# Performance work log

Measured on AMD Instinct MI355X. Metric: run time of the kernel, lower is better.

## Reference

```python
import jax, jax.numpy as jnp
import numpy as np

N = 50000        # nodes
E = 800000       # edges (avg degree 16)
NODE_DIM = 64
HID = 64
OUT = 1
K = 2            # hops per TAGConv
P = 0.5          # dropout rate


def setup_inputs() -> dict:
    key = jax.random.key(0)
    ks = jax.random.split(key, 8)
    x = jax.random.normal(ks[0], (N, NODE_DIM), dtype=jnp.float32)
    edge_index = jax.random.randint(ks[1], (2, E), 0, N, dtype=jnp.int64)
    # positive edge weights (traffic-style), keeps degree normalization well-defined
    edge_attr = jax.random.uniform(ks[2], (E,), dtype=jnp.float32, minval=0.1, maxval=1.0)
    s = 0.1
    W0 = (jax.random.normal(ks[3], (K + 1, NODE_DIM, HID), dtype=jnp.float32) * s)
    W1 = (jax.random.normal(ks[4], (K + 1, HID, HID), dtype=jnp.float32) * s)
    W2 = (jax.random.normal(ks[5], (K + 1, HID, OUT), dtype=jnp.float32) * s)
    a0 = jnp.full((1,), 0.25, dtype=jnp.float32)  # PReLU slope (num_parameters=1)
    a1 = jnp.full((1,), 0.25, dtype=jnp.float32)
    return {"x": x, "edge_index": edge_index, "edge_attr": edge_attr,
            "W0": W0, "W1": W1, "W2": W2, "a0": a0, "a1": a1}


def _tagconv(x, row, col, norm, W):
    # out = sum_{k=0..K} (A_norm^k x) @ W[k]
    out = x @ W[0]
    h = x
    for k in range(1, K + 1):
        # gather source features, scale by edge norm, scatter-add to targets
        h = jax.ops.segment_sum(h[row] * norm[:, None], col, num_segments=N)
        out = out + h @ W[k]
    return out


def _dropout(h, key):
    keep = jax.random.bernoulli(key, 1.0 - P, h.shape)
    return jnp.where(keep, h / (1.0 - P), 0.0)


def _prelu(h, a):
    return jnp.where(h >= 0, h, a * h)


def reference(x, edge_index, edge_attr, W0, W1, W2, a0, a1):
    row, col = edge_index[0], edge_index[1]
    # symmetric GCN normalization (PyG TAGConv default, no added self-loops)
    deg = jax.ops.segment_sum(edge_attr, col, num_segments=N)
    dinv = jnp.where(deg > 0, jax.lax.rsqrt(jnp.maximum(deg, 1e-12)), 0.0)
    norm = dinv[row] * edge_attr * dinv[col]

    dk = jax.random.split(jax.random.key(42), 2)
    h = _tagconv(x, row, col, norm, W0)
    h = _prelu(_dropout(h, dk[0]), a0)
    h = _tagconv(h, row, col, norm, W1)
    h = _prelu(_dropout(h, dk[1]), a1)
    return _tagconv(h, row, col, norm, W2)
```

## Files before the change

### kernel.cpp

```cpp
#include <hip/hip_runtime.h>
#include <stdint.h>

#define N_NODES 50000
#define N_EDGES 800000
#define DIM 64
#define FEAT_TOTAL (N_NODES * DIM)
#define ELL_S 48
#define NB 200
#define BROWS 250
#define BCAP 6000
#define ECHUNK (N_EDGES / NB)
#define AST 200

typedef __attribute__((ext_vector_type(8))) short bf16x8;
typedef __attribute__((ext_vector_type(4))) float f32x4;

__device__ inline float bf2f(uint32_t h) { return __uint_as_float(h << 16); }
__device__ inline uint32_t f2bf(float f) {
  uint32_t u = __float_as_uint(f);
  return (u + 0x7fffu + ((u >> 16) & 1u)) >> 16;
}

__host__ __device__ inline void threefry2x32(uint32_t k0, uint32_t k1,
                                             uint32_t x0, uint32_t x1,
                                             uint32_t& o0, uint32_t& o1) {
  uint32_t ks[3] = {k0, k1, k0 ^ k1 ^ 0x1BD11BDAu};
  x0 += ks[0];
  x1 += ks[1];
  const uint32_t R[2][4] = {{13u, 15u, 26u, 6u}, {17u, 29u, 16u, 24u}};
#pragma unroll
  for (int g = 0; g < 5; ++g) {
    const uint32_t* r = R[g & 1];
#pragma unroll
    for (int j = 0; j < 4; ++j) {
      x0 += x1;
      x1 = (x1 << r[j]) | (x1 >> (32u - r[j]));
      x1 ^= x0;
    }
    x0 += ks[(g + 1) % 3];
    x1 += ks[(g + 2) % 3] + (uint32_t)(g + 1);
  }
  o0 = x0;
  o1 = x1;
}

__global__ __launch_bounds__(256) void phaseA(
    const int* __restrict__ row, const int* __restrict__ col,
    const float* __restrict__ w, int* __restrict__ bfill,
    int2* __restrict__ bkt, int E) {
  __shared__ int hist[NB], base[NB], off[NB];
  int t = threadIdx.x;
  int lo = blockIdx.x * ECHUNK;
  int hi = min(lo + ECHUNK, E);
  for (int i = t; i < NB; i += 256) hist[i] = 0;
  __syncthreads();
  for (int e = lo + t; e < hi; e += 256) atomicAdd(&hist[col[e] / BROWS], 1);
  __syncthreads();
  for (int i = t; i < NB; i += 256) {
    base[i] = atomicAdd(&bfill[i], hist[i]);
    off[i] = 0;
  }
  __syncthreads();
  for (int e = lo + t; e < hi; e += 256) {
    int c = col[e];
    int bin = c / BROWS;
    int rank = atomicAdd(&off[bin], 1);
    int dest = base[bin] + rank;
    if (dest < BCAP) {
      int2 ent;
      ent.x = row[e] | ((c - bin * BROWS) << 17);
      ent.y = __float_as_int(w[e]);
      bkt[(size_t)bin * BCAP + dest] = ent;
    }
  }
}

__global__ __launch_bounds__(256) void phaseC(
    const int* __restrict__ bfill, const int2* __restrict__ bkt,
    int2* __restrict__ ell, int* __restrict__ cnt, float* __restrict__ deg) {
  __shared__ int lcnt[BROWS];
  __shared__ float ldeg[BROWS];
  int t = threadIdx.x;
  int b = blockIdx.x;
  for (int i = t; i < BROWS; i += 256) {
    lcnt[i] = 0;
    ldeg[i] = 0.0f;
  }
  __syncthreads();
  int sz = min(bfill[b], BCAP);
  const int2* src = bkt + (size_t)b * BCAP;
  for (int i = t; i < sz; i += 256) {
    int2 ent = src[i];
    int cl = (ent.x >> 17) & 0xff;
    int r = ent.x & 0x1ffff;
    float wv = __int_as_float(ent.y);
    int slot = atomicAdd(&lcnt[cl], 1);
    if (slot < ELL_S) {
      int2 o;
      o.x = r;
      o.y = ent.y;
      ell[(size_t)(b * BROWS + cl) * ELL_S + slot] = o;
    }
    atomicAdd(&ldeg[cl], wv);
  }
  __syncthreads();
  for (int i = t; i < BROWS; i += 256) {
    cnt[b * BROWS + i] = lcnt[i];
    deg[b * BROWS + i] = ldeg[i];
  }
}

__global__ void dinv_kernel(float* __restrict__ d_io, int n) {
  int i = blockIdx.x * blockDim.x + threadIdx.x;
  if (i >= n) return;
  float d = d_io[i];
  d_io[i] = (d > 0.0f) ? rsqrtf(fmaxf(d, 1e-12f)) : 0.0f;
}

__global__ void normw_ell(int2* __restrict__ ell, const int* __restrict__ cnt,
                          const float* __restrict__ dinv, int n_nodes) {
  int gid = blockIdx.x * blockDim.x + threadIdx.x;
  int n = gid >> 6;
  if (n >= n_nodes) return;
  int lane = threadIdx.x & 63;
  int c = min(cnt[n], ELL_S);
  if (lane >= c) return;
  float dn = dinv[n];
  int2 ent = ell[(size_t)n * ELL_S + lane];
  ent.y = __float_as_int(dinv[ent.x] * __int_as_float(ent.y) * dn);
  ell[(size_t)n * ELL_S + lane] = ent;
}

__global__ void cvt_wt(const float* __restrict__ W0, const float* __restrict__ W1,
                       uint16_t* __restrict__ Wt0, uint16_t* __restrict__ Wt1) {
  int id = blockIdx.x * blockDim.x + threadIdx.x;
  if (id >= 192 * DIM) return;
  int kk = id >> 6;
  int j = id & 63;
  Wt0[j * 192 + kk] = (uint16_t)f2bf(W0[id]);
  Wt1[j * 192 + kk] = (uint16_t)f2bf(W1[id]);
}

__global__ void prop_f32(const float* __restrict__ src,
                         uint16_t* __restrict__ dst,
                         const int2* __restrict__ ell,
                         const int* __restrict__ cnt, int n_nodes) {
  int gid = blockIdx.x * blockDim.x + threadIdx.x;
  int n = gid >> 6;
  if (n >= n_nodes) return;
  int lane = threadIdx.x & 63;
  int eg = lane >> 4;
  int fc = lane & 15;
  int c = min(cnt[n], ELL_S);
  const int2* p = ell + (size_t)n * ELL_S;
  float4 acc = {0.f, 0.f, 0.f, 0.f};
  int k = eg;
  for (; k + 4 < c; k += 8) {
    int2 e0 = p[k];
    int2 e1 = p[k + 4];
    float w0 = __int_as_float(e0.y);
    float w1 = __int_as_float(e1.y);
    float4 v0 = *(const float4*)&src[e0.x * DIM + fc * 4];
    float4 v1 = *(const float4*)&src[e1.x * DIM + fc * 4];
    acc.x += v0.x * w0 + v1.x * w1;
    acc.y += v0.y * w0 + v1.y * w1;
    acc.z += v0.z * w0 + v1.z * w1;
    acc.w += v0.w * w0 + v1.w * w1;
  }
  if (k < c) {
    int2 e0 = p[k];
    float w0 = __int_as_float(e0.y);
    float4 v = *(const float4*)&src[e0.x * DIM + fc * 4];
    acc.x += v.x * w0;
    acc.y += v.y * w0;
    acc.z += v.z * w0;
    acc.w += v.w * w0;
  }
#pragma unroll
  for (int m = 16; m <= 32; m <<= 1) {
    acc.x += __shfl_xor(acc.x, m);
    acc.y += __shfl_xor(acc.y, m);
    acc.z += __shfl_xor(acc.z, m);
    acc.w += __shfl_xor(acc.w, m);
  }
  if (eg == 0) {
    uint2 r;
    r.x = f2bf(acc.x) | (f2bf(acc.y) << 16);
    r.y = f2bf(acc.z) | (f2bf(acc.w) << 16);
    *(uint2*)&dst[(size_t)n * DIM + fc * 4] = r;
  }
}

__global__ void prop_bf16(const uint16_t* __restrict__ src,
                          uint16_t* __restrict__ dst,
                          const int2* __restrict__ ell,
                          const int* __restrict__ cnt, int n_nodes) {
  int gid = blockIdx.x * blockDim.x + threadIdx.x;
  int n = gid >> 5;
  if (n >= n_nodes) return;
  int hl = threadIdx.x & 31;
  int eg = hl >> 3;
  int fc = hl & 7;
  int c = min(cnt[n], ELL_S);
  const int2* p = ell + (size_t)n * ELL_S;
  float acc[8] = {0.f, 0.f, 0.f, 0.f, 0.f, 0.f, 0.f, 0.f};
  int k = eg;
  for (; k + 4 < c; k += 8) {
    int2 e0 = p[k];
    int2 e1 = p[k + 4];
    float w0 = __int_as_float(e0.y);
    float w1 = __int_as_float(e1.y);
    uint4 v0 = *(const uint4*)&src[e0.x * DIM + fc * 8];
    uint4 v1 = *(const uint4*)&src[e1.x * DIM + fc * 8];
    acc[0] += bf2f(v0.x & 0xffffu) * w0 + bf2f(v1.x & 0xffffu) * w1;
    acc[1] += bf2f(v0.x >> 16) * w0 + bf2f(v1.x >> 16) * w1;
    acc[2] += bf2f(v0.y & 0xffffu) * w0 + bf2f(v1.y & 0xffffu) * w1;
    acc[3] += bf2f(v0.y >> 16) * w0 + bf2f(v1.y >> 16) * w1;
    acc[4] += bf2f(v0.z & 0xffffu) * w0 + bf2f(v1.z & 0xffffu) * w1;
    acc[5] += bf2f(v0.z >> 16) * w0 + bf2f(v1.z >> 16) * w1;
    acc[6] += bf2f(v0.w & 0xffffu) * w0 + bf2f(v1.w & 0xffffu) * w1;
    acc[7] += bf2f(v0.w >> 16) * w0 + bf2f(v1.w >> 16) * w1;
  }
  if (k < c) {
    int2 e0 = p[k];
    float w0 = __int_as_float(e0.y);
    uint4 v0 = *(const uint4*)&src[e0.x * DIM + fc * 8];
    acc[0] += bf2f(v0.x & 0xffffu) * w0;
    acc[1] += bf2f(v0.x >> 16) * w0;
    acc[2] += bf2f(v0.y & 0xffffu) * w0;
    acc[3] += bf2f(v0.y >> 16) * w0;
    acc[4] += bf2f(v0.z & 0xffffu) * w0;
    acc[5] += bf2f(v0.z >> 16) * w0;
    acc[6] += bf2f(v0.w & 0xffffu) * w0;
    acc[7] += bf2f(v0.w >> 16) * w0;
  }
#pragma unroll
  for (int m = 8; m <= 16; m <<= 1) {
#pragma unroll
    for (int j = 0; j < 8; ++j) acc[j] += __shfl_xor(acc[j], m);
  }
  if (eg == 0) {
    uint4 r;
    r.x = f2bf(acc[0]) | (f2bf(acc[1]) << 16);
    r.y = f2bf(acc[2]) | (f2bf(acc[3]) << 16);
    r.z = f2bf(acc[4]) | (f2bf(acc[5]) << 16);
    r.w = f2bf(acc[6]) | (f2bf(acc[7]) << 16);
    *(uint4*)&dst[(size_t)n * DIM + fc * 8] = r;
  }
}

__global__ void sprop_add_ell(const float* __restrict__ src,
                              const float* __restrict__ addv,
                              float* __restrict__ dst,
                              const int2* __restrict__ ell,
                              const int* __restrict__ cnt, int n_nodes) {
  int n = blockIdx.x * blockDim.x + threadIdx.x;
  if (n >= n_nodes) return;
  int c = min(cnt[n], ELL_S);
  const int2* p = ell + (size_t)n * ELL_S;
  float acc = addv[n];
  for (int k = 0; k < c; ++k)
    acc += __int_as_float(p[k].y) * src[p[k].x];
  dst[n] = acc;
}

template <bool XF32>
__global__ __launch_bounds__(256) void gemm3_mfma(
    const void* Xv, const uint16_t* __restrict__ P1,
    const uint16_t* __restrict__ P2, const uint16_t* __restrict__ Wt,
    uint16_t* out, int n_nodes, uint32_t k0, uint32_t k1,
    const float* __restrict__ a) {
  __shared__ uint16_t sA[64 * AST];
  __shared__ uint16_t sB[64 * AST];
  int t = threadIdx.x;
  int n0 = blockIdx.x * 64;
  if (XF32) {
    const float* X = (const float*)Xv;
#pragma unroll
    for (int it = 0; it < 2; ++it) {
      int chunk = t + it * 256;
      int rrow = chunk >> 3;
      int cc = chunk & 7;
      int nc = min(n0 + rrow, n_nodes - 1);
      const float* s = &X[(size_t)nc * DIM + cc * 8];
      float4 v0 = *(const float4*)s;
      float4 v1 = *(const float4*)(s + 4);
      uint16_t* d = &sA[rrow * AST + cc * 8];
      d[0] = (uint16_t)f2bf(v0.x);
      d[1] = (uint16_t)f2bf(v0.y);
      d[2] = (uint16_t)f2bf(v0.z);
      d[3] = (uint16_t)f2bf(v0.w);
      d[4] = (uint16_t)f2bf(v1.x);
      d[5] = (uint16_t)f2bf(v1.y);
      d[6] = (uint16_t)f2bf(v1.z);
      d[7] = (uint16_t)f2bf(v1.w);
    }
  } else {
    const uint16_t* X = (const uint16_t*)Xv;
#pragma unroll
    for (int it = 0; it < 2; ++it) {
      int chunk = t + it * 256;
      int rrow = chunk >> 3;
      int cc = chunk & 7;
      int nc = min(n0 + rrow, n_nodes - 1);
      uint4 v = *(const uint4*)&X[(size_t)nc * DIM + cc * 8];
      *(uint4*)&sA[rrow * AST + cc * 8] = v;
    }
  }
#pragma unroll
  for (int m = 1; m < 3; ++m) {
    const uint16_t* S = (m == 1) ? P1 : P2;
#pragma unroll
    for (int it = 0; it < 2; ++it) {
      int chunk = t + it * 256;
      int rrow = chunk >> 3;
      int cc = chunk & 7;
      int nc = min(n0 + rrow, n_nodes - 1);
      uint4 v = *(const uint4*)&S[(size_t)nc * DIM + cc * 8];
      *(uint4*)&sA[rrow * AST + m * DIM + cc * 8] = v;
    }
  }
#pragma unroll
  for (int it = 0; it < 6; ++it) {
    int chunk = t + it * 256;
    int rrow = chunk / 24;
    int cc = chunk % 24;
    uint4 v = *(const uint4*)&Wt[rrow * 192 + cc * 8];
    *(uint4*)&sB[rrow * AST + cc * 8] = v;
  }
  __syncthreads();
  int wv = t >> 6;
  int lane = t & 63;
  int lm = lane & 15;
  int quad = lane >> 4;
  f32x4 acc[4] = {};
  const uint16_t* pB = &sB[(wv * 16 + lm) * AST + quad * 8];
  const uint16_t* pA = &sA[lm * AST + quad * 8];
#pragma unroll
  for (int ks = 0; ks < 6; ++ks) {
    bf16x8 bf = *(const bf16x8*)(pB + ks * 32);
#pragma unroll
    for (int rt = 0; rt < 4; ++rt) {
      bf16x8 af = *(const bf16x8*)(pA + rt * 16 * AST + ks * 32);
      acc[rt] = __builtin_amdgcn_mfma_f32_16x16x32_bf16(af, bf, acc[rt], 0, 0, 0);
    }
  }
  float al = a[0];
  int col = wv * 16 + lm;
#pragma unroll
  for (int rt = 0; rt < 4; ++rt) {
#pragma unroll
    for (int r = 0; r < 4; ++r) {
      int n = n0 + rt * 16 + quad * 4 + r;
      if (n < n_nodes) {
        float v = acc[rt][r];
        uint32_t idx = (uint32_t)(n * DIM + col);
        uint32_t o0, o1;
        threefry2x32(k0, k1, 0u, idx, o0, o1);
        v = ((o0 ^ o1) & 0x80000000u) ? 0.0f : (v + v);
        v = (v >= 0.0f) ? v : al * v;
        out[(size_t)n * DIM + col] = (uint16_t)f2bf(v);
      }
    }
  }
}

__global__ void matvec3_bf16(const uint16_t* __restrict__ F,
                             const float* __restrict__ W2,
                             float* __restrict__ y0, float* __restrict__ y1,
                             float* __restrict__ y2, int n_nodes) {
  int gid = blockIdx.x * blockDim.x + threadIdx.x;
  int n = gid >> 6;
  int i = gid & 63;
  if (n >= n_nodes) return;
  float v = bf2f((uint32_t)F[(size_t)n * DIM + i]);
  float s0 = v * W2[i], s1 = v * W2[DIM + i], s2 = v * W2[2 * DIM + i];
#pragma unroll
  for (int off = 32; off > 0; off >>= 1) {
    s0 += __shfl_down(s0, off);
    s1 += __shfl_down(s1, off);
    s2 += __shfl_down(s2, off);
  }
  if (i == 0) {
    y0[n] = s0;
    y1[n] = s1;
    y2[n] = s2;
  }
}

extern "C" void kernel_launch(void* const* d_in, const int* in_sizes, int n_in,
                              void* d_out, int out_size, void* d_ws,
                              size_t ws_size, hipStream_t stream) {
  const float* x = (const float*)d_in[0];
  const int* ei = (const int*)d_in[1];
  const float* ew = (const float*)d_in[2];
  const float* W0 = (const float*)d_in[3];
  const float* W1 = (const float*)d_in[4];
  const float* W2 = (const float*)d_in[5];
  const float* a0 = (const float*)d_in[6];
  const float* a1 = (const float*)d_in[7];
  float* out = (float*)d_out;

  const int* row = ei;
  const int* col = ei + N_EDGES;

  const size_t need = (size_t)(2 * N_NODES + 256) * 4 +
                      (size_t)NB * BCAP * 8 + (size_t)N_NODES * ELL_S * 8 +
                      (size_t)(2 * 192 * DIM) * 2 +
                      (size_t)(3 * FEAT_TOTAL) * 2 + (size_t)(4 * N_NODES) * 4;
  if (ws_size < need) return;
  float* deg = (float*)d_ws;
  int* cnt = (int*)(deg + N_NODES);
  int* bfill = cnt + N_NODES;
  int2* bkt = (int2*)(bfill + 256);
  int2* ell = bkt + (size_t)NB * BCAP;
  uint16_t* Wt0 = (uint16_t*)(ell + (size_t)N_NODES * ELL_S);
  uint16_t* Wt1 = Wt0 + 192 * DIM;
  uint16_t* F0 = Wt1 + 192 * DIM;
  uint16_t* F1 = F0 + FEAT_TOTAL;
  uint16_t* F2 = F1 + FEAT_TOTAL;
  float* y0 = (float*)(F2 + FEAT_TOTAL);
  float* y1 = y0 + N_NODES;
  float* y2 = y1 + N_NODES;
  float* z1 = y2 + N_NODES;

  uint32_t dk0_0, dk0_1, dk1_0, dk1_1;
  threefry2x32(0u, 42u, 0u, 0u, dk0_0, dk0_1);
  threefry2x32(0u, 42u, 0u, 1u, dk1_0, dk1_1);

  const int BLK = 256;
  const int gridN = (N_NODES + BLK - 1) / BLK;
  const int gridNF = (FEAT_TOTAL + BLK - 1) / BLK;
  const int gridNH = (N_NODES * 32 + BLK - 1) / BLK;
  const int gridT = (N_NODES + 63) / 64;

  hipMemsetAsync(bfill, 0, 256 * sizeof(int), stream);
  phaseA<<<NB, BLK, 0, stream>>>(row, col, ew, bfill, bkt, N_EDGES);
  phaseC<<<NB, BLK, 0, stream>>>(bfill, bkt, ell, cnt, deg);
  dinv_kernel<<<gridN, BLK, 0, stream>>>(deg, N_NODES);
  normw_ell<<<gridNF, BLK, 0, stream>>>(ell, cnt, deg, N_NODES);
  cvt_wt<<<48, BLK, 0, stream>>>(W0, W1, Wt0, Wt1);

  prop_f32<<<gridNF, BLK, 0, stream>>>(x, F1, ell, cnt, N_NODES);
  prop_bf16<<<gridNH, BLK, 0, stream>>>(F1, F2, ell, cnt, N_NODES);
  gemm3_mfma<true><<<gridT, BLK, 0, stream>>>(x, F1, F2, Wt0, F0, N_NODES,
                                              dk0_0, dk0_1, a0);
  prop_bf16<<<gridNH, BLK, 0, stream>>>(F0, F1, ell, cnt, N_NODES);
  prop_bf16<<<gridNH, BLK, 0, stream>>>(F1, F2, ell, cnt, N_NODES);
  gemm3_mfma<false><<<gridT, BLK, 0, stream>>>(F0, F1, F2, Wt1, F0, N_NODES,
                                               dk1_0, dk1_1, a1);
  matvec3_bf16<<<gridNF, BLK, 0, stream>>>(F0, W2, y0, y1, y2, N_NODES);
  sprop_add_ell<<<gridN, BLK, 0, stream>>>(y2, y1, z1, ell, cnt, N_NODES);
  sprop_add_ell<<<gridN, BLK, 0, stream>>>(z1, y0, out, ell, cnt, N_NODES);
}
```

Before: 262.7 us.

## Fuse second-hop gather into MFMA GEMM and pre-convert input features to bf16

The second propagation hop of each TAGConv layer now runs inside the GEMM kernel. Each block gathers its 64 nodes' neighbour features straight into shared memory, so the F2 buffer is never written to or read back from global memory and one launch per layer disappears. The input x is converted to bf16 up front so the first hop can reuse the bf16 propagation kernel instead of the fp32 one. The dinv computation is folded into phaseC and the weight conversion is merged with the x conversion. In exchange, the gather inside the GEMM runs with far fewer threads and an LDS-heavy block, so its latency hiding may be weaker than in the standalone propagation kernel.

After: 301.5 us. 1.15x slower.

```diff
diff --git a/kernel.cpp b/kernel.cpp
--- a/kernel.cpp
+++ b/kernel.cpp
@@ -77,7 +77,7 @@
 
 __global__ __launch_bounds__(256) void phaseC(
     const int* __restrict__ bfill, const int2* __restrict__ bkt,
-    int2* __restrict__ ell, int* __restrict__ cnt, float* __restrict__ deg) {
+    int2* __restrict__ ell, int* __restrict__ cnt, float* __restrict__ dinv) {
   __shared__ int lcnt[BROWS];
   __shared__ float ldeg[BROWS];
   int t = threadIdx.x;
@@ -106,15 +106,9 @@
   __syncthreads();
   for (int i = t; i < BROWS; i += 256) {
     cnt[b * BROWS + i] = lcnt[i];
-    deg[b * BROWS + i] = ldeg[i];
-  }
-}
-
-__global__ void dinv_kernel(float* __restrict__ d_io, int n) {
-  int i = blockIdx.x * blockDim.x + threadIdx.x;
-  if (i >= n) return;
-  float d = d_io[i];
-  d_io[i] = (d > 0.0f) ? rsqrtf(fmaxf(d, 1e-12f)) : 0.0f;
+    float d = ldeg[i];
+    dinv[b * BROWS + i] = (d > 0.0f) ? rsqrtf(fmaxf(d, 1e-12f)) : 0.0f;
+  }
 }
 
 __global__ void normw_ell(int2* __restrict__ ell, const int* __restrict__ cnt,
@@ -131,63 +125,18 @@
   ell[(size_t)n * ELL_S + lane] = ent;
 }
 
-__global__ void cvt_wt(const float* __restrict__ W0, const float* __restrict__ W1,
-                       uint16_t* __restrict__ Wt0, uint16_t* __restrict__ Wt1) {
+__global__ void cvt_all(const float* __restrict__ x,
+                        const float* __restrict__ W0,
+                        const float* __restrict__ W1,
+                        uint16_t* __restrict__ xb, uint16_t* __restrict__ Wt0,
+                        uint16_t* __restrict__ Wt1) {
   int id = blockIdx.x * blockDim.x + threadIdx.x;
-  if (id >= 192 * DIM) return;
-  int kk = id >> 6;
-  int j = id & 63;
-  Wt0[j * 192 + kk] = (uint16_t)f2bf(W0[id]);
-  Wt1[j * 192 + kk] = (uint16_t)f2bf(W1[id]);
-}
-
-__global__ void prop_f32(const float* __restrict__ src,
-                         uint16_t* __restrict__ dst,
-                         const int2* __restrict__ ell,
-                         const int* __restrict__ cnt, int n_nodes) {
-  int gid = blockIdx.x * blockDim.x + threadIdx.x;
-  int n = gid >> 6;
-  if (n >= n_nodes) return;
-  int lane = threadIdx.x & 63;
-  int eg = lane >> 4;
-  int fc = lane & 15;
-  int c = min(cnt[n], ELL_S);
-  const int2* p = ell + (size_t)n * ELL_S;
-  float4 acc = {0.f, 0.f, 0.f, 0.f};
-  int k = eg;
-  for (; k + 4 < c; k += 8) {
-    int2 e0 = p[k];
-    int2 e1 = p[k + 4];
-    float w0 = __int_as_float(e0.y);
-    float w1 = __int_as_float(e1.y);
-    float4 v0 = *(const float4*)&src[e0.x * DIM + fc * 4];
-    float4 v1 = *(const float4*)&src[e1.x * DIM + fc * 4];
-    acc.x += v0.x * w0 + v1.x * w1;
-    acc.y += v0.y * w0 + v1.y * w1;
-    acc.z += v0.z * w0 + v1.z * w1;
-    acc.w += v0.w * w0 + v1.w * w1;
-  }
-  if (k < c) {
-    int2 e0 = p[k];
-    float w0 = __int_as_float(e0.y);
-    float4 v = *(const float4*)&src[e0.x * DIM + fc * 4];
-    acc.x += v.x * w0;
-    acc.y += v.y * w0;
-    acc.z += v.z * w0;
-    acc.w += v.w * w0;
-  }
-#pragma unroll
-  for (int m = 16; m <= 32; m <<= 1) {
-    acc.x += __shfl_xor(acc.x, m);
-    acc.y += __shfl_xor(acc.y, m);
-    acc.z += __shfl_xor(acc.z, m);
-    acc.w += __shfl_xor(acc.w, m);
-  }
-  if (eg == 0) {
-    uint2 r;
-    r.x = f2bf(acc.x) | (f2bf(acc.y) << 16);
-    r.y = f2bf(acc.z) | (f2bf(acc.w) << 16);
-    *(uint2*)&dst[(size_t)n * DIM + fc * 4] = r;
+  if (id < FEAT_TOTAL) xb[id] = (uint16_t)f2bf(x[id]);
+  if (id < 192 * DIM) {
+    int kk = id >> 6;
+    int j = id & 63;
+    Wt0[j * 192 + kk] = (uint16_t)f2bf(W0[id]);
+    Wt1[j * 192 + kk] = (uint16_t)f2bf(W1[id]);
   }
 }
 
@@ -264,52 +213,18 @@
   dst[n] = acc;
 }
 
-template <bool XF32>
-__global__ __launch_bounds__(256) void gemm3_mfma(
-    const void* Xv, const uint16_t* __restrict__ P1,
-    const uint16_t* __restrict__ P2, const uint16_t* __restrict__ Wt,
-    uint16_t* out, int n_nodes, uint32_t k0, uint32_t k1,
-    const float* __restrict__ a) {
+__global__ __launch_bounds__(256) void gemm3_mfma_g(
+    const uint16_t* X, const uint16_t* __restrict__ P1,
+    const int2* __restrict__ ell, const int* __restrict__ cnt,
+    const uint16_t* __restrict__ Wt, uint16_t* out, int n_nodes, uint32_t k0,
+    uint32_t k1, const float* __restrict__ a) {
   __shared__ uint16_t sA[64 * AST];
   __shared__ uint16_t sB[64 * AST];
   int t = threadIdx.x;
   int n0 = blockIdx.x * 64;
-  if (XF32) {
-    const float* X = (const float*)Xv;
-#pragma unroll
-    for (int it = 0; it < 2; ++it) {
-      int chunk = t + it * 256;
-      int rrow = chunk >> 3;
-      int cc = chunk & 7;
-      int nc = min(n0 + rrow, n_nodes - 1);
-      const float* s = &X[(size_t)nc * DIM + cc * 8];
-      float4 v0 = *(const float4*)s;
-      float4 v1 = *(const float4*)(s + 4);
-      uint16_t* d = &sA[rrow * AST + cc * 8];
-      d[0] = (uint16_t)f2bf(v0.x);
-      d[1] = (uint16_t)f2bf(v0.y);
-      d[2] = (uint16_t)f2bf(v0.z);
-      d[3] = (uint16_t)f2bf(v0.w);
-      d[4] = (uint16_t)f2bf(v1.x);
-      d[5] = (uint16_t)f2bf(v1.y);
-      d[6] = (uint16_t)f2bf(v1.z);
-      d[7] = (uint16_t)f2bf(v1.w);
-    }
-  } else {
-    const uint16_t* X = (const uint16_t*)Xv;
-#pragma unroll
-    for (int it = 0; it < 2; ++it) {
-      int chunk = t + it * 256;
-      int rrow = chunk >> 3;
-      int cc = chunk & 7;
-      int nc = min(n0 + rrow, n_nodes - 1);
-      uint4 v = *(const uint4*)&X[(size_t)nc * DIM + cc * 8];
-      *(uint4*)&sA[rrow * AST + cc * 8] = v;
-    }
-  }
-#pragma unroll
-  for (int m = 1; m < 3; ++m) {
-    const uint16_t* S = (m == 1) ? P1 : P2;
+#pragma unroll
+  for (int m = 0; m < 2; ++m) {
+    const uint16_t* S = (m == 0) ? X : P1;
 #pragma unroll
     for (int it = 0; it < 2; ++it) {
       int chunk = t + it * 256;
@@ -318,6 +233,65 @@
       int nc = min(n0 + rrow, n_nodes - 1);
       uint4 v = *(const uint4*)&S[(size_t)nc * DIM + cc * 8];
       *(uint4*)&sA[rrow * AST + m * DIM + cc * 8] = v;
+    }
+  }
+  {
+    int wv = t >> 6;
+    int lane = t & 63;
+    int half = lane >> 5;
+    int hl = lane & 31;
+    int eg = hl >> 3;
+    int fc = hl & 7;
+#pragma unroll
+    for (int i = 0; i < 8; ++i) {
+      int ln = wv * 16 + i * 2 + half;
+      int nc = min(n0 + ln, n_nodes - 1);
+      int c = min(cnt[nc], ELL_S);
+      const int2* p = ell + (size_t)nc * ELL_S;
+      float acc[8] = {0.f, 0.f, 0.f, 0.f, 0.f, 0.f, 0.f, 0.f};
+      int k = eg;
+      for (; k + 4 < c; k += 8) {
+        int2 e0 = p[k];
+        int2 e1 = p[k + 4];
+        float w0 = __int_as_float(e0.y);
+        float w1 = __int_as_float(e1.y);
+        uint4 v0 = *(const uint4*)&P1[e0.x * DIM + fc * 8];
+        uint4 v1 = *(const uint4*)&P1[e1.x * DIM + fc * 8];
+        acc[0] += bf2f(v0.x & 0xffffu) * w0 + bf2f(v1.x & 0xffffu) * w1;
+        acc[1] += bf2f(v0.x >> 16) * w0 + bf2f(v1.x >> 16) * w1;
+        acc[2] += bf2f(v0.y & 0xffffu) * w0 + bf2f(v1.y & 0xffffu) * w1;
+        acc[3] += bf2f(v0.y >> 16) * w0 + bf2f(v1.y >> 16) * w1;
+        acc[4] += bf2f(v0.z & 0xffffu) * w0 + bf2f(v1.z & 0xffffu) * w1;
+        acc[5] += bf2f(v0.z >> 16) * w0 + bf2f(v1.z >> 16) * w1;
+        acc[6] += bf2f(v0.w & 0xffffu) * w0 + bf2f(v1.w & 0xffffu) * w1;
+        acc[7] += bf2f(v0.w >> 16) * w0 + bf2f(v1.w >> 16) * w1;
+      }
+      if (k < c) {
+        int2 e0 = p[k];
+        float w0 = __int_as_float(e0.y);
+        uint4 v0 = *(const uint4*)&P1[e0.x * DIM + fc * 8];
+        acc[0] += bf2f(v0.x & 0xffffu) * w0;
+        acc[1] += bf2f(v0.x >> 16) * w0;
+        acc[2] += bf2f(v0.y & 0xffffu) * w0;
+        acc[3] += bf2f(v0.y >> 16) * w0;
+        acc[4] += bf2f(v0.z & 0xffffu) * w0;
+        acc[5] += bf2f(v0.z >> 16) * w0;
+        acc[6] += bf2f(v0.w & 0xffffu) * w0;
+        acc[7] += bf2f(v0.w >> 16) * w0;
+      }
+#pragma unroll
+      for (int m = 8; m <= 16; m <<= 1) {
+#pragma unroll
+        for (int j = 0; j < 8; ++j) acc[j] += __shfl_xor(acc[j], m);
+      }
+      if (eg == 0) {
+        uint4 r;
+        r.x = f2bf(acc[0]) | (f2bf(acc[1]) << 16);
+        r.y = f2bf(acc[2]) | (f2bf(acc[3]) << 16);
+        r.z = f2bf(acc[4]) | (f2bf(acc[5]) << 16);
+        r.w = f2bf(acc[6]) | (f2bf(acc[7]) << 16);
+        *(uint4*)&sA[ln * AST + 2 * DIM + fc * 8] = r;
+      }
     }
   }
 #pragma unroll
@@ -409,17 +383,17 @@
                       (size_t)(2 * 192 * DIM) * 2 +
                       (size_t)(3 * FEAT_TOTAL) * 2 + (size_t)(4 * N_NODES) * 4;
   if (ws_size < need) return;
-  float* deg = (float*)d_ws;
-  int* cnt = (int*)(deg + N_NODES);
+  float* dinv = (float*)d_ws;
+  int* cnt = (int*)(dinv + N_NODES);
   int* bfill = cnt + N_NODES;
   int2* bkt = (int2*)(bfill + 256);
   int2* ell = bkt + (size_t)NB * BCAP;
   uint16_t* Wt0 = (uint16_t*)(ell + (size_t)N_NODES * ELL_S);
   uint16_t* Wt1 = Wt0 + 192 * DIM;
-  uint16_t* F0 = Wt1 + 192 * DIM;
+  uint16_t* xb = Wt1 + 192 * DIM;
+  uint16_t* F0 = xb + FEAT_TOTAL;
   uint16_t* F1 = F0 + FEAT_TOTAL;
-  uint16_t* F2 = F1 + FEAT_TOTAL;
-  float* y0 = (float*)(F2 + FEAT_TOTAL);
+  float* y0 = (float*)(F1 + FEAT_TOTAL);
   float* y1 = y0 + N_NODES;
   float* y2 = y1 + N_NODES;
   float* z1 = y2 + N_NODES;
@@ -436,19 +410,16 @@
 
   hipMemsetAsync(bfill, 0, 256 * sizeof(int), stream);
   phaseA<<<NB, BLK, 0, stream>>>(row, col, ew, bfill, bkt, N_EDGES);
-  phaseC<<<NB, BLK, 0, stream>>>(bfill, bkt, ell, cnt, deg);
-  dinv_kernel<<<gridN, BLK, 0, stream>>>(deg, N_NODES);
-  normw_ell<<<gridNF, BLK, 0, stream>>>(ell, cnt, deg, N_NODES);
-  cvt_wt<<<48, BLK, 0, stream>>>(W0, W1, Wt0, Wt1);
-
-  prop_f32<<<gridNF, BLK, 0, stream>>>(x, F1, ell, cnt, N_NODES);
-  prop_bf16<<<gridNH, BLK, 0, stream>>>(F1, F2, ell, cnt, N_NODES);
-  gemm3_mfma<true><<<gridT, BLK, 0, stream>>>(x, F1, F2, Wt0, F0, N_NODES,
-                                              dk0_0, dk0_1, a0);
+  phaseC<<<NB, BLK, 0, stream>>>(bfill, bkt, ell, cnt, dinv);
+  normw_ell<<<gridNF, BLK, 0, stream>>>(ell, cnt, dinv, N_NODES);
+  cvt_all<<<gridNF, BLK, 0, stream>>>(x, W0, W1, xb, Wt0, Wt1);
+
+  prop_bf16<<<gridNH, BLK, 0, stream>>>(xb, F1, ell, cnt, N_NODES);
+  gemm3_mfma_g<<<gridT, BLK, 0, stream>>>(xb, F1, ell, cnt, Wt0, F0, N_NODES,
+                                          dk0_0, dk0_1, a0);
   prop_bf16<<<gridNH, BLK, 0, stream>>>(F0, F1, ell, cnt, N_NODES);
-  prop_bf16<<<gridNH, BLK, 0, stream>>>(F1, F2, ell, cnt, N_NODES);
-  gemm3_mfma<false><<<gridT, BLK, 0, stream>>>(F0, F1, F2, Wt1, F0, N_NODES,
-                                               dk1_0, dk1_1, a1);
+  gemm3_mfma_g<<<gridT, BLK, 0, stream>>>(F0, F1, ell, cnt, Wt1, F0, N_NODES,
+                                          dk1_0, dk1_1, a1);
   matvec3_bf16<<<gridNF, BLK, 0, stream>>>(F0, W2, y0, y1, y2, N_NODES);
   sprop_add_ell<<<gridN, BLK, 0, stream>>>(y2, y1, z1, ell, cnt, N_NODES);
   sprop_add_ell<<<gridN, BLK, 0, stream>>>(z1, y0, out, ell, cnt, N_NODES);
```
